# Kernel tuning notes

Measured on AMD Instinct MI355X. Metric: run time of the kernel, lower is better.

## Reference

```python
import jax, jax.numpy as jnp
import numpy as np

NEG = -1e9  # mask value for non-edges (matches masked_fill(-inf) numerically-safely)
SLOPE = 0.2  # LeakyReLU negative slope in GraphAttentionLayer


def gat_layer(x, W, a_l, a_r, adj, n_heads):
    """One GraphAttentionLayer (eval mode, is_concat=True).
    e[i,j,h] = leakyrelu(a_l . g[i,h] + a_r . g[j,h])  (attn Linear split into halves)
    softmax over j masked by adj, then aggregate neighbors.
    """
    n = x.shape[0]
    g = (x @ W).reshape(n, n_heads, -1)          # [n, h, f]
    el = jnp.einsum('ihf,f->ih', g, a_l)          # score contribution of node i
    er = jnp.einsum('jhf,f->jh', g, a_r)          # score contribution of node j
    e = jax.nn.leaky_relu(el[:, None, :] + er[None, :, :], SLOPE)  # [n, n, h]
    e = jnp.where(adj[:, :, None] != 0, e, NEG)
    a = jax.nn.softmax(e, axis=1)                 # softmax over neighbors j
    out = jnp.einsum('ijh,jhf->ihf', a, g)        # weighted aggregation
    return out.reshape(n, -1)                     # concat heads


def setup_inputs() -> dict:
    key = jax.random.key(0)
    ks = jax.random.split(key, 8)
    N, IN, HID, OUT, H = 2048, 512, 256, 128, 8
    x = jax.random.normal(ks[0], (N, IN), dtype=jnp.float32)
    adj = jax.random.randint(ks[1], (N, N), 0, 2, dtype=jnp.int32)
    adj = adj.at[jnp.arange(N), jnp.arange(N)].set(1)  # self loops: no empty softmax rows
    s = 0.05
    W1 = jax.random.normal(ks[2], (IN, HID), dtype=jnp.float32) * s
    a1_l = jax.random.normal(ks[3], (HID // H,), dtype=jnp.float32) * s
    a1_r = jax.random.normal(ks[4], (HID // H,), dtype=jnp.float32) * s
    W2 = jax.random.normal(ks[5], (HID, OUT), dtype=jnp.float32) * s
    a2_l = jax.random.normal(ks[6], (OUT,), dtype=jnp.float32) * s
    a2_r = jax.random.normal(ks[7], (OUT,), dtype=jnp.float32) * s
    return {"x": x, "W1": W1, "a1_l": a1_l, "a1_r": a1_r,
            "W2": W2, "a2_l": a2_l, "a2_r": a2_r, "adj_mat": adj}


def reference(x, W1, a1_l, a1_r, W2, a2_l, a2_r, adj_mat):
    # eval mode: nn.Dropout is identity
    h = gat_layer(x, W1, a1_l, a1_r, adj_mat, n_heads=8)
    h = jax.nn.elu(h)
    out = gat_layer(h, W2, a2_l, a2_r, adj_mat, n_heads=1)
    return out
```

## Files before the change

kernel.cpp:

```cpp
#include <hip/hip_runtime.h>
#include <hip/hip_bf16.h>

#define NN 2048
typedef unsigned short u16;
typedef unsigned long long u64;
typedef __attribute__((ext_vector_type(8))) short short8;
typedef __attribute__((ext_vector_type(4))) float f32x4;

__device__ __forceinline__ unsigned bfb(float x) {
    unsigned u = __float_as_uint(x);
    return (u + 0x7FFFu + ((u >> 16) & 1u)) >> 16;
}
__device__ __forceinline__ unsigned pk2(float a, float b) {
    unsigned r;
    asm("v_cvt_pk_bf16_f32 %0, %1, %2" : "=v"(r) : "v"(a), "v"(b));
    return r;
}

__global__ __launch_bounds__(256) void gemm1(const float* __restrict__ x,
                                             const float* __restrict__ W1,
                                             const int* __restrict__ adj,
                                             const float* __restrict__ al,
                                             const float* __restrict__ ar,
                                             u16* __restrict__ GT,
                                             float* __restrict__ el,
                                             float* __restrict__ ert,
                                             u64* __restrict__ ab) {
    const int rt = blockIdx.x, cs = blockIdx.y;
    const int i0 = rt * 16;
    const int t = threadIdx.x, lane = t & 63, w = t >> 6;
    const int q = lane >> 4, n = lane & 15;
    const int ct = w & 1, kh = w >> 1;
    __shared__ __align__(16) u16 As[16][520];
    __shared__ __align__(16) u16 Bs[32][520];
    __shared__ float osh[2][16][16];
    __shared__ float pel[2][16], per_[2][16];

    const int b = cs * 128 + rt;
    const int u0 = b * 64 + w * 16;
    int av[16];
#pragma unroll
    for (int it = 0; it < 16; ++it) {
        int u = u0 + it;
        av[it] = adj[(size_t)(u >> 5) * NN + (u & 31) * 64 + lane];
    }

    {
        const float4* xs = (const float4*)(x + (size_t)i0 * 512);
#pragma unroll
        for (int j = 0; j < 8; ++j) {
            float4 v = xs[j * 256 + t];
            int off = (j * 256 + t) * 4;
            int r = off >> 9, k = off & 511;
            uint2 o;
            o.x = pk2(v.x, v.y);
            o.y = pk2(v.z, v.w);
            *(uint2*)&As[r][k ^ ((r & 7) << 3)] = o;
        }
    }
    {
        const int c4 = (t & 7) * 4, kq = t >> 3;
#pragma unroll 8
        for (int pass = 0; pass < 16; ++pass) {
            int k = pass * 32 + kq;
            float4 v = *(const float4*)(W1 + (size_t)k * 256 + cs * 32 + c4);
            Bs[c4 + 0][k ^ (((c4 + 0) & 7) << 3)] = (u16)bfb(v.x);
            Bs[c4 + 1][k ^ (((c4 + 1) & 7) << 3)] = (u16)bfb(v.y);
            Bs[c4 + 2][k ^ (((c4 + 2) & 7) << 3)] = (u16)bfb(v.z);
            Bs[c4 + 3][k ^ (((c4 + 3) & 7) << 3)] = (u16)bfb(v.w);
        }
    }
#pragma unroll
    for (int it = 0; it < 16; ++it) {
        u64 mk = __ballot(av[it] != 0);
        int u = u0 + it;
        if (lane == 0) ab[(size_t)(u >> 5) * 32 + (u & 31)] = mk;
    }
    __syncthreads();

    const int an = n, bn = ct * 16 + n;
    const int k0 = kh * 256 + q * 8;
    f32x4 acc = {0.f, 0.f, 0.f, 0.f};
#pragma unroll
    for (int ks = 0; ks < 8; ++ks) {
        short8 a = *(const short8*)&As[an][(k0 + ks * 32) ^ ((an & 7) << 3)];
        short8 bb = *(const short8*)&Bs[bn][(k0 + ks * 32) ^ ((bn & 7) << 3)];
        acc = __builtin_amdgcn_mfma_f32_16x16x32_bf16(a, bb, acc, 0, 0, 0);
    }
    if (kh == 1) {
#pragma unroll
        for (int r = 0; r < 4; ++r) osh[ct][q * 4 + r][n] = acc[r];
    }
    __syncthreads();
    if (kh == 0) {
#pragma unroll
        for (int r = 0; r < 4; ++r) acc[r] += osh[ct][q * 4 + r][n];
        uint2 g0;
        g0.x = pk2(acc[0], acc[1]);
        g0.y = pk2(acc[2], acc[3]);
        *(uint2*)&GT[(size_t)(cs * 32 + ct * 16 + n) * NN + i0 + q * 4] = g0;
        const float alv = al[ct * 16 + n], arv = ar[ct * 16 + n];
#pragma unroll
        for (int r = 0; r < 4; ++r) {
            float ve = acc[r] * alv, vr = acc[r] * arv;
#pragma unroll
            for (int off = 1; off <= 8; off <<= 1) {
                ve += __shfl_xor(ve, off);
                vr += __shfl_xor(vr, off);
            }
            if (n == 0) { pel[ct][q * 4 + r] = ve; per_[ct][q * 4 + r] = vr; }
        }
    }
    __syncthreads();
    if (t < 16) {
        el[(size_t)(i0 + t) * 8 + cs] = pel[0][t] + pel[1][t];
        ert[(size_t)cs * NN + i0 + t] = per_[0][t] + per_[1][t];
    }
}

__global__ __launch_bounds__(256) void gemm2(const u16* __restrict__ A,
                                             const float* __restrict__ W2,
                                             const float* __restrict__ al,
                                             const float* __restrict__ ar,
                                             u16* __restrict__ GT,
                                             float* __restrict__ el2p,
                                             float* __restrict__ er2p) {
    const int i0 = blockIdx.x * 16, cs = blockIdx.y;
    const int t = threadIdx.x, lane = t & 63, w = t >> 6;
    const int q = lane >> 4, n = lane & 15;
    const int ct = w & 1, kh = w >> 1;
    __shared__ __align__(16) u16 As[16][264];
    __shared__ __align__(16) u16 Bs[32][264];
    __shared__ float osh[2][16][16];
    __shared__ float pel[2][16], per_[2][16];

    {
        const uint2* hs = (const uint2*)(A + (size_t)i0 * 256);
#pragma unroll
        for (int j = 0; j < 4; ++j) {
            uint2 v = hs[j * 256 + t];
            int off = (j * 256 + t) * 4;
            int r = off >> 8, k = off & 255;
            *(uint2*)&As[r][k ^ ((r & 7) << 3)] = v;
        }
    }
    {
        const int c4 = (t & 7) * 4, kq = t >> 3;
#pragma unroll 8
        for (int pass = 0; pass < 8; ++pass) {
            int k = pass * 32 + kq;
            float4 v = *(const float4*)(W2 + (size_t)k * 128 + cs * 32 + c4);
            Bs[c4 + 0][k ^ (((c4 + 0) & 7) << 3)] = (u16)bfb(v.x);
            Bs[c4 + 1][k ^ (((c4 + 1) & 7) << 3)] = (u16)bfb(v.y);
            Bs[c4 + 2][k ^ (((c4 + 2) & 7) << 3)] = (u16)bfb(v.z);
            Bs[c4 + 3][k ^ (((c4 + 3) & 7) << 3)] = (u16)bfb(v.w);
        }
    }
    __syncthreads();

    const int an = n, bn = ct * 16 + n;
    const int k0 = kh * 128 + q * 8;
    f32x4 acc = {0.f, 0.f, 0.f, 0.f};
#pragma unroll
    for (int ks = 0; ks < 4; ++ks) {
        short8 a = *(const short8*)&As[an][(k0 + ks * 32) ^ ((an & 7) << 3)];
        short8 bb = *(const short8*)&Bs[bn][(k0 + ks * 32) ^ ((bn & 7) << 3)];
        acc = __builtin_amdgcn_mfma_f32_16x16x32_bf16(a, bb, acc, 0, 0, 0);
    }
    if (kh == 1) {
#pragma unroll
        for (int r = 0; r < 4; ++r) osh[ct][q * 4 + r][n] = acc[r];
    }
    __syncthreads();
    if (kh == 0) {
#pragma unroll
        for (int r = 0; r < 4; ++r) acc[r] += osh[ct][q * 4 + r][n];
        uint2 g0;
        g0.x = pk2(acc[0], acc[1]);
        g0.y = pk2(acc[2], acc[3]);
        *(uint2*)&GT[(size_t)(cs * 32 + ct * 16 + n) * NN + i0 + q * 4] = g0;
        const float alv = al[cs * 32 + ct * 16 + n], arv = ar[cs * 32 + ct * 16 + n];
#pragma unroll
        for (int r = 0; r < 4; ++r) {
            float ve = acc[r] * alv, vr = acc[r] * arv;
#pragma unroll
            for (int off = 1; off <= 8; off <<= 1) {
                ve += __shfl_xor(ve, off);
                vr += __shfl_xor(vr, off);
            }
            if (n == 0) { pel[ct][q * 4 + r] = ve; per_[ct][q * 4 + r] = vr; }
        }
    }
    __syncthreads();
    if (t < 16) {
        el2p[(size_t)cs * NN + i0 + t] = pel[0][t] + pel[1][t];
        er2p[(size_t)cs * NN + i0 + t] = per_[0][t] + per_[1][t];
    }
}

__global__ __launch_bounds__(512, 4) void attn1(const float* __restrict__ el,
                                                const float* __restrict__ ert,
                                                const unsigned* __restrict__ ab32,
                                                const u16* __restrict__ gbt,
                                                u16* __restrict__ hbb) {
    const int rt = blockIdx.x, sec = blockIdx.y;
    const int i0 = rt * 16, h0 = sec * 2;
    const int t = threadIdx.x, lane = t & 63, w = t >> 6;
    const int q = lane >> 4, n = lane & 15;
    const int m = t >> 5, jq = t & 31;
    const int hl = w >> 2, ch = (w >> 1) & 1, kf2 = w & 1;

    __shared__ u16 ersb[2][2048];
    __shared__ __align__(16) u16 pl[2][2][16][264];
    __shared__ unsigned absh[16][64];
    __shared__ float psum_sh[16][2];
    __shared__ float osh[2][2][16][16];
    __shared__ float wmax[2][8];
    __shared__ float mxsh[2];

    float4 v0 = *(const float4*)(ert + (size_t)h0 * NN + t * 4);
    float4 v1 = *(const float4*)(ert + (size_t)(h0 + 1) * NN + t * 4);
    uint2 c0, c1;
    c0.x = pk2(v0.x, v0.y); c0.y = pk2(v0.z, v0.w);
    c1.x = pk2(v1.x, v1.y); c1.y = pk2(v1.z, v1.w);
    *(uint2*)&ersb[0][t * 4] = c0;
    *(uint2*)&ersb[1][t * 4] = c1;
    float m0 = fmaxf(fmaxf(v0.x, v0.y), fmaxf(v0.z, v0.w));
    float m1 = fmaxf(fmaxf(v1.x, v1.y), fmaxf(v1.z, v1.w));
#pragma unroll
    for (int off = 32; off; off >>= 1) {
        m0 = fmaxf(m0, __shfl_xor(m0, off));
        m1 = fmaxf(m1, __shfl_xor(m1, off));
    }
    if (lane == 0) { wmax[0][w] = m0; wmax[1][w] = m1; }
    for (int c = t; c < 1024; c += 512)
        absh[c >> 6][c & 63] = ab32[(size_t)(i0 + (c >> 6)) * 64 + (c & 63)];
    __syncthreads();
    if (t < 2) {
        float mm = wmax[t][0];
#pragma unroll
        for (int ww = 1; ww < 8; ++ww) mm = fmaxf(mm, wmax[t][ww]);
        mxsh[t] = mm;
    }
    __syncthreads();

    float elv[2], mxv[2], ps[2];
#pragma unroll
    for (int h = 0; h < 2; ++h) {
        float e = el[(size_t)(i0 + m) * 8 + h0 + h];
        elv[h] = e;
        float mm = e + mxsh[h];
        mxv[h] = fmaxf(mm, 0.2f * mm);
        ps[h] = 0.f;
    }

    auto stage = [&](int tl, int nb) {
#pragma unroll
        for (int sub = 0; sub < 2; ++sub) {
            unsigned word = absh[m][tl * 8 + sub * 4 + (jq >> 3)];
            unsigned bits = (word >> ((jq & 7) * 4)) & 0xFu;
            const int jo = tl * 256 + sub * 128 + jq * 4;
            uint2 raw0 = *(const uint2*)&ersb[0][jo];
            uint2 raw1 = *(const uint2*)&ersb[1][jo];
#pragma unroll
            for (int h = 0; h < 2; ++h) {
                uint2 raw = h ? raw1 : raw0;
                float e0 = __uint_as_float(raw.x << 16);
                float e1 = __uint_as_float(raw.x & 0xFFFF0000u);
                float e2 = __uint_as_float(raw.y << 16);
                float e3 = __uint_as_float(raw.y & 0xFFFF0000u);
                float s0 = elv[h] + e0, s1 = elv[h] + e1, s2 = elv[h] + e2, s3 = elv[h] + e3;
                s0 = fmaxf(s0, 0.2f * s0) - mxv[h];
                s1 = fmaxf(s1, 0.2f * s1) - mxv[h];
                s2 = fmaxf(s2, 0.2f * s2) - mxv[h];
                s3 = fmaxf(s3, 0.2f * s3) - mxv[h];
                float p0 = (bits & 1u) ? __expf(s0) : 0.f;
                float p1 = (bits & 2u) ? __expf(s1) : 0.f;
                float p2 = (bits & 4u) ? __expf(s2) : 0.f;
                float p3 = (bits & 8u) ? __expf(s3) : 0.f;
                ps[h] += (p0 + p1) + (p2 + p3);
                uint2 pkv;
                pkv.x = pk2(p0, p1);
                pkv.y = pk2(p2, p3);
                *(uint2*)&pl[nb][h][m][sub * 128 + jq * 4] = pkv;
            }
        }
    };

    const int col = sec * 64 + hl * 32 + ch * 16 + n;
    const u16* gb = gbt + (size_t)col * NN + kf2 * 128 + q * 8;
    short8 bc0 = *(const short8*)gb;
    short8 bc1 = *(const short8*)(gb + 32);
    short8 bc2 = *(const short8*)(gb + 64);
    short8 bc3 = *(const short8*)(gb + 96);
    f32x4 acc = {0.f, 0.f, 0.f, 0.f};

    stage(0, 0);
    __syncthreads();

    for (int tile = 0; tile < 8; ++tile) {
        short8 bn0 = bc0, bn1 = bc1, bn2 = bc2, bn3 = bc3;
        if (tile < 7) {
            const u16* gq = gb + (tile + 1) * 256;
            bn0 = *(const short8*)gq;
            bn1 = *(const short8*)(gq + 32);
            bn2 = *(const short8*)(gq + 64);
            bn3 = *(const short8*)(gq + 96);
        }
        const u16* ap = &pl[tile & 1][hl][n][kf2 * 128 + q * 8];
        short8 a0 = *(const short8*)ap;
        short8 a1 = *(const short8*)(ap + 32);
        short8 a2 = *(const short8*)(ap + 64);
        short8 a3 = *(const short8*)(ap + 96);
        acc = __builtin_amdgcn_mfma_f32_16x16x32_bf16(a0, bc0, acc, 0, 0, 0);
        acc = __builtin_amdgcn_mfma_f32_16x16x32_bf16(a1, bc1, acc, 0, 0, 0);
        acc = __builtin_amdgcn_mfma_f32_16x16x32_bf16(a2, bc2, acc, 0, 0, 0);
        acc = __builtin_amdgcn_mfma_f32_16x16x32_bf16(a3, bc3, acc, 0, 0, 0);
        if (tile < 7) stage(tile + 1, (tile + 1) & 1);
        bc0 = bn0; bc1 = bn1; bc2 = bn2; bc3 = bn3;
        __syncthreads();
    }

#pragma unroll
    for (int h = 0; h < 2; ++h) {
        float v = ps[h];
#pragma unroll
        for (int off = 16; off; off >>= 1) v += __shfl_down(v, off, 32);
        if (jq == 0) psum_sh[m][h] = v;
    }
    if (kf2 == 1) {
#pragma unroll
        for (int r = 0; r < 4; ++r) osh[hl][ch][q * 4 + r][n] = acc[r];
    }
    __syncthreads();
    if (kf2 == 0) {
#pragma unroll
        for (int r = 0; r < 4; ++r) {
            int mr = q * 4 + r;
            float o = (acc[r] + osh[hl][ch][mr][n]) / psum_sh[mr][hl];
            o = o > 0.f ? o : (__expf(o) - 1.f);
            hbb[(size_t)(i0 + mr) * 256 + col] = (u16)bfb(o);
        }
    }
}

__global__ __launch_bounds__(512) void attn2(const float* __restrict__ el2p,
                                             const float* __restrict__ er2p,
                                             const unsigned* __restrict__ ab32,
                                             const u16* __restrict__ gbt,
                                             float* __restrict__ out) {
    const int rt = blockIdx.x, sec = blockIdx.y;
    const int i0 = rt * 16;
    const int t = threadIdx.x, lane = t & 63, w = t >> 6;
    const int q = lane >> 4, n = lane & 15;
    const int m = t >> 5, jq = t & 31;
    const int ct = w >> 1, kf2 = w & 1;

    __shared__ u16 ersb[2048];
    __shared__ __align__(16) u16 pl[2][16][264];
    __shared__ unsigned absh[16][64];
    __shared__ float psum_sh[16];
    __shared__ float osh[4][16][16];
    __shared__ float wmax[8];
    __shared__ float mxsh;

    float4 a0 = *(const float4*)(er2p + t * 4);
    float4 a1 = *(const float4*)(er2p + NN + t * 4);
    float4 a2 = *(const float4*)(er2p + 2 * NN + t * 4);
    float4 a3 = *(const float4*)(er2p + 3 * NN + t * 4);
    float4 v0;
    v0.x = ((a0.x + a1.x) + (a2.x + a3.x));
    v0.y = ((a0.y + a1.y) + (a2.y + a3.y));
    v0.z = ((a0.z + a1.z) + (a2.z + a3.z));
    v0.w = ((a0.w + a1.w) + (a2.w + a3.w));
    uint2 c0;
    c0.x = pk2(v0.x, v0.y); c0.y = pk2(v0.z, v0.w);
    *(uint2*)&ersb[t * 4] = c0;
    float m0 = fmaxf(fmaxf(v0.x, v0.y), fmaxf(v0.z, v0.w));
#pragma unroll
    for (int off = 32; off; off >>= 1) m0 = fmaxf(m0, __shfl_xor(m0, off));
    if (lane == 0) wmax[w] = m0;
    for (int c = t; c < 1024; c += 512)
        absh[c >> 6][c & 63] = ab32[(size_t)(i0 + (c >> 6)) * 64 + (c & 63)];
    __syncthreads();
    if (t == 0) {
        float mm = wmax[0];
#pragma unroll
        for (int ww = 1; ww < 8; ++ww) mm = fmaxf(mm, wmax[ww]);
        mxsh = mm;
    }
    __syncthreads();

    const float elv = el2p[i0 + m] + el2p[NN + i0 + m] + el2p[2 * NN + i0 + m] + el2p[3 * NN + i0 + m];
    float mm2 = elv + mxsh;
    const float mxv = fmaxf(mm2, 0.2f * mm2);
    float ps = 0.f;

    auto stage = [&](int tl, int nb) {
#pragma unroll
        for (int sub = 0; sub < 2; ++sub) {
            unsigned word = absh[m][tl * 8 + sub * 4 + (jq >> 3)];
            unsigned bits = (word >> ((jq & 7) * 4)) & 0xFu;
            const int jo = tl * 256 + sub * 128 + jq * 4;
            uint2 raw = *(const uint2*)&ersb[jo];
            float e0 = __uint_as_float(raw.x << 16);
            float e1 = __uint_as_float(raw.x & 0xFFFF0000u);
            float e2 = __uint_as_float(raw.y << 16);
            float e3 = __uint_as_float(raw.y & 0xFFFF0000u);
            float s0 = elv + e0, s1 = elv + e1, s2 = elv + e2, s3 = elv + e3;
            s0 = fmaxf(s0, 0.2f * s0) - mxv;
            s1 = fmaxf(s1, 0.2f * s1) - mxv;
            s2 = fmaxf(s2, 0.2f * s2) - mxv;
            s3 = fmaxf(s3, 0.2f * s3) - mxv;
            float p0 = (bits & 1u) ? __expf(s0) : 0.f;
            float p1 = (bits & 2u) ? __expf(s1) : 0.f;
            float p2 = (bits & 4u) ? __expf(s2) : 0.f;
            float p3 = (bits & 8u) ? __expf(s3) : 0.f;
            ps += (p0 + p1) + (p2 + p3);
            uint2 pkv;
            pkv.x = pk2(p0, p1);
            pkv.y = pk2(p2, p3);
            *(uint2*)&pl[nb][m][sub * 128 + jq * 4] = pkv;
        }
    };

    const int col = sec * 64 + ct * 16 + n;
    const u16* gb = gbt + (size_t)col * NN + kf2 * 128 + q * 8;
    short8 bc0 = *(const short8*)gb;
    short8 bc1 = *(const short8*)(gb + 32);
    short8 bc2 = *(const short8*)(gb + 64);
    short8 bc3 = *(const short8*)(gb + 96);
    f32x4 acc = {0.f, 0.f, 0.f, 0.f};

    stage(0, 0);
    __syncthreads();

    for (int tile = 0; tile < 8; ++tile) {
        short8 bn0 = bc0, bn1 = bc1, bn2 = bc2, bn3 = bc3;
        if (tile < 7) {
            const u16* gq = gb + (tile + 1) * 256;
            bn0 = *(const short8*)gq;
            bn1 = *(const short8*)(gq + 32);
            bn2 = *(const short8*)(gq + 64);
            bn3 = *(const short8*)(gq + 96);
        }
        const u16* ap = &pl[tile & 1][n][kf2 * 128 + q * 8];
        short8 a0v = *(const short8*)ap;
        short8 a1v = *(const short8*)(ap + 32);
        short8 a2v = *(const short8*)(ap + 64);
        short8 a3v = *(const short8*)(ap + 96);
        acc = __builtin_amdgcn_mfma_f32_16x16x32_bf16(a0v, bc0, acc, 0, 0, 0);
        acc = __builtin_amdgcn_mfma_f32_16x16x32_bf16(a1v, bc1, acc, 0, 0, 0);
        acc = __builtin_amdgcn_mfma_f32_16x16x32_bf16(a2v, bc2, acc, 0, 0, 0);
        acc = __builtin_amdgcn_mfma_f32_16x16x32_bf16(a3v, bc3, acc, 0, 0, 0);
        if (tile < 7) stage(tile + 1, (tile + 1) & 1);
        bc0 = bn0; bc1 = bn1; bc2 = bn2; bc3 = bn3;
        __syncthreads();
    }

#pragma unroll
    for (int off = 16; off; off >>= 1) ps += __shfl_down(ps, off, 32);
    if (jq == 0) psum_sh[m] = ps;
    if (kf2 == 1) {
#pragma unroll
        for (int r = 0; r < 4; ++r) osh[ct][q * 4 + r][n] = acc[r];
    }
    __syncthreads();
    if (kf2 == 0) {
#pragma unroll
        for (int r = 0; r < 4; ++r) {
            int mr = q * 4 + r;
            out[(size_t)(i0 + mr) * 128 + col] = (acc[r] + osh[ct][mr][n]) / psum_sh[mr];
        }
    }
}

extern "C" void kernel_launch(void* const* d_in, const int* in_sizes, int n_in,
                              void* d_out, int out_size, void* d_ws, size_t ws_size,
                              hipStream_t stream) {
    const float* x   = (const float*)d_in[0];
    const float* W1  = (const float*)d_in[1];
    const float* a1l = (const float*)d_in[2];
    const float* a1r = (const float*)d_in[3];
    const float* W2  = (const float*)d_in[4];
    const float* a2l = (const float*)d_in[5];
    const float* a2r = (const float*)d_in[6];
    const int* adj = (const int*)d_in[7];

    char* p = (char*)d_ws;
    unsigned* abits = (unsigned*)p;  p += (size_t)NN * 64 * 4;
    u16* gbt1  = (u16*)p;            p += (size_t)256 * NN * 2;
    u16* hbb   = (u16*)p;            p += (size_t)NN * 256 * 2;
    u16* gbt2  = (u16*)p;            p += (size_t)128 * NN * 2;
    float* el1 = (float*)p;          p += (size_t)NN * 8 * 4;
    float* ert1 = (float*)p;         p += (size_t)8 * NN * 4;
    float* el2p = (float*)p;         p += (size_t)4 * NN * 4;
    float* er2p = (float*)p;         p += (size_t)4 * NN * 4;

    gemm1<<<dim3(128, 8), 256, 0, stream>>>(x, W1, adj, a1l, a1r, gbt1, el1, ert1, (u64*)abits);
    attn1<<<dim3(128, 4), 512, 0, stream>>>(el1, ert1, abits, gbt1, hbb);

    gemm2<<<dim3(128, 4), 256, 0, stream>>>(hbb, W2, a2l, a2r, gbt2, el2p, er2p);
    attn2<<<dim3(128, 2), 512, 0, stream>>>(el2p, er2p, abits, gbt2, (float*)d_out);
}
```

Baseline: 123.8 us.

## Drop adjacency bitmask precompute, read int adj directly in attention; XCD-aware block mapping

Removes the ballot-based bitmask packing of the adjacency matrix in gemm1, so each attention kernel reads the raw int32 adjacency rows directly and builds the 4-bit masks in registers. Adds an XCD-aware remapping of block indices so that blocks sharing rows or sections land on the same chiplet's L2. It also folds log2(e) into the attention vectors so the softmax can use the raw v_exp_f32 instead of __expf. The trade is reading 16 MB of int adjacency in each of the two attention kernels, instead of a 0.5 MB bitmask, in exchange for removing the mask-building pass from gemm1.

```diff
diff --git a/kernel.cpp b/kernel.cpp
--- a/kernel.cpp
+++ b/kernel.cpp
@@ -16,17 +16,24 @@
     asm("v_cvt_pk_bf16_f32 %0, %1, %2" : "=v"(r) : "v"(a), "v"(b));
     return r;
 }
+__device__ __forceinline__ float ex2(float x) {
+    float r;
+    asm("v_exp_f32 %0, %1" : "=v"(r) : "v"(x));
+    return r;
+}
+
+#define LOG2E 1.4426950408889634f
 
 __global__ __launch_bounds__(256) void gemm1(const float* __restrict__ x,
                                              const float* __restrict__ W1,
-                                             const int* __restrict__ adj,
                                              const float* __restrict__ al,
                                              const float* __restrict__ ar,
                                              u16* __restrict__ GT,
                                              float* __restrict__ el,
-                                             float* __restrict__ ert,
-                                             u64* __restrict__ ab) {
-    const int rt = blockIdx.x, cs = blockIdx.y;
+                                             float* __restrict__ ert) {
+    const int bid = blockIdx.x;
+    const int xcd = bid & 7, idx = bid >> 3;
+    const int rt = xcd * 16 + (idx & 15), cs = idx >> 4;
     const int i0 = rt * 16;
     const int t = threadIdx.x, lane = t & 63, w = t >> 6;
     const int q = lane >> 4, n = lane & 15;
@@ -36,22 +43,13 @@
     __shared__ float osh[2][16][16];
     __shared__ float pel[2][16], per_[2][16];
 
-    const int b = cs * 128 + rt;
-    const int u0 = b * 64 + w * 16;
-    int av[16];
-#pragma unroll
-    for (int it = 0; it < 16; ++it) {
-        int u = u0 + it;
-        av[it] = adj[(size_t)(u >> 5) * NN + (u & 31) * 64 + lane];
-    }
-
     {
         const float4* xs = (const float4*)(x + (size_t)i0 * 512);
 #pragma unroll
         for (int j = 0; j < 8; ++j) {
             float4 v = xs[j * 256 + t];
-            int off = (j * 256 + t) * 4;
-            int r = off >> 9, k = off & 511;
+            int e = (j * 256 + t) * 4;
+            int r = e >> 9, k = e & 511;
             uint2 o;
             o.x = pk2(v.x, v.y);
             o.y = pk2(v.z, v.w);
@@ -70,12 +68,6 @@
             Bs[c4 + 3][k ^ (((c4 + 3) & 7) << 3)] = (u16)bfb(v.w);
         }
     }
-#pragma unroll
-    for (int it = 0; it < 16; ++it) {
-        u64 mk = __ballot(av[it] != 0);
-        int u = u0 + it;
-        if (lane == 0) ab[(size_t)(u >> 5) * 32 + (u & 31)] = mk;
-    }
     __syncthreads();
 
     const int an = n, bn = ct * 16 + n;
@@ -99,7 +91,7 @@
         g0.x = pk2(acc[0], acc[1]);
         g0.y = pk2(acc[2], acc[3]);
         *(uint2*)&GT[(size_t)(cs * 32 + ct * 16 + n) * NN + i0 + q * 4] = g0;
-        const float alv = al[ct * 16 + n], arv = ar[ct * 16 + n];
+        const float alv = al[ct * 16 + n] * LOG2E, arv = ar[ct * 16 + n] * LOG2E;
 #pragma unroll
         for (int r = 0; r < 4; ++r) {
             float ve = acc[r] * alv, vr = acc[r] * arv;
@@ -139,8 +131,8 @@
 #pragma unroll
         for (int j = 0; j < 4; ++j) {
             uint2 v = hs[j * 256 + t];
-            int off = (j * 256 + t) * 4;
-            int r = off >> 8, k = off & 255;
+            int e = (j * 256 + t) * 4;
+            int r = e >> 8, k = e & 255;
             *(uint2*)&As[r][k ^ ((r & 7) << 3)] = v;
         }
     }
@@ -179,7 +171,7 @@
         g0.x = pk2(acc[0], acc[1]);
         g0.y = pk2(acc[2], acc[3]);
         *(uint2*)&GT[(size_t)(cs * 32 + ct * 16 + n) * NN + i0 + q * 4] = g0;
-        const float alv = al[cs * 32 + ct * 16 + n], arv = ar[cs * 32 + ct * 16 + n];
+        const float alv = al[cs * 32 + ct * 16 + n] * LOG2E, arv = ar[cs * 32 + ct * 16 + n] * LOG2E;
 #pragma unroll
         for (int r = 0; r < 4; ++r) {
             float ve = acc[r] * alv, vr = acc[r] * arv;
@@ -200,10 +192,13 @@
 
 __global__ __launch_bounds__(512, 4) void attn1(const float* __restrict__ el,
                                                 const float* __restrict__ ert,
-                                                const unsigned* __restrict__ ab32,
+                                                const int* __restrict__ adj,
                                                 const u16* __restrict__ gbt,
                                                 u16* __restrict__ hbb) {
-    const int rt = blockIdx.x, sec = blockIdx.y;
+    const int bid = blockIdx.x;
+    const int xcd = bid & 7, idx = bid >> 3;
+    const int sec = xcd >> 1;
+    const int rt = (xcd & 1) * 64 + idx;
     const int i0 = rt * 16, h0 = sec * 2;
     const int t = threadIdx.x, lane = t & 63, w = t >> 6;
     const int q = lane >> 4, n = lane & 15;
@@ -212,7 +207,6 @@
 
     __shared__ u16 ersb[2][2048];
     __shared__ __align__(16) u16 pl[2][2][16][264];
-    __shared__ unsigned absh[16][64];
     __shared__ float psum_sh[16][2];
     __shared__ float osh[2][2][16][16];
     __shared__ float wmax[2][8];
@@ -233,8 +227,6 @@
         m1 = fmaxf(m1, __shfl_xor(m1, off));
     }
     if (lane == 0) { wmax[0][w] = m0; wmax[1][w] = m1; }
-    for (int c = t; c < 1024; c += 512)
-        absh[c >> 6][c & 63] = ab32[(size_t)(i0 + (c >> 6)) * 64 + (c & 63)];
     __syncthreads();
     if (t < 2) {
         float mm = wmax[t][0];
@@ -253,12 +245,16 @@
         mxv[h] = fmaxf(mm, 0.2f * mm);
         ps[h] = 0.f;
     }
+    const int* adjrow = adj + (size_t)(i0 + m) * NN;
 
     auto stage = [&](int tl, int nb) {
+        int4 av0 = *(const int4*)(adjrow + tl * 256 + jq * 4);
+        int4 av1 = *(const int4*)(adjrow + tl * 256 + 128 + jq * 4);
 #pragma unroll
         for (int sub = 0; sub < 2; ++sub) {
-            unsigned word = absh[m][tl * 8 + sub * 4 + (jq >> 3)];
-            unsigned bits = (word >> ((jq & 7) * 4)) & 0xFu;
+            int4 av = sub ? av1 : av0;
+            unsigned bits = (unsigned)(av.x != 0) | ((unsigned)(av.y != 0) << 1) |
+                            ((unsigned)(av.z != 0) << 2) | ((unsigned)(av.w != 0) << 3);
             const int jo = tl * 256 + sub * 128 + jq * 4;
             uint2 raw0 = *(const uint2*)&ersb[0][jo];
             uint2 raw1 = *(const uint2*)&ersb[1][jo];
@@ -274,10 +270,10 @@
                 s1 = fmaxf(s1, 0.2f * s1) - mxv[h];
                 s2 = fmaxf(s2, 0.2f * s2) - mxv[h];
                 s3 = fmaxf(s3, 0.2f * s3) - mxv[h];
-                float p0 = (bits & 1u) ? __expf(s0) : 0.f;
-                float p1 = (bits & 2u) ? __expf(s1) : 0.f;
-                float p2 = (bits & 4u) ? __expf(s2) : 0.f;
-                float p3 = (bits & 8u) ? __expf(s3) : 0.f;
+                float p0 = (bits & 1u) ? ex2(s0) : 0.f;
+                float p1 = (bits & 2u) ? ex2(s1) : 0.f;
+                float p2 = (bits & 4u) ? ex2(s2) : 0.f;
+                float p3 = (bits & 8u) ? ex2(s3) : 0.f;
                 ps[h] += (p0 + p1) + (p2 + p3);
                 uint2 pkv;
                 pkv.x = pk2(p0, p1);
@@ -346,10 +342,13 @@
 
 __global__ __launch_bounds__(512) void attn2(const float* __restrict__ el2p,
                                              const float* __restrict__ er2p,
-                                             const unsigned* __restrict__ ab32,
+                                             const int* __restrict__ adj,
                                              const u16* __restrict__ gbt,
                                              float* __restrict__ out) {
-    const int rt = blockIdx.x, sec = blockIdx.y;
+    const int bid = blockIdx.x;
+    const int xcd = bid & 7, idx = bid >> 3;
+    const int sec = xcd >> 2;
+    const int rt = (xcd & 3) * 32 + idx;
     const int i0 = rt * 16;
     const int t = threadIdx.x, lane = t & 63, w = t >> 6;
     const int q = lane >> 4, n = lane & 15;
@@ -358,7 +357,6 @@
 
     __shared__ u16 ersb[2048];
     __shared__ __align__(16) u16 pl[2][16][264];
-    __shared__ unsigned absh[16][64];
     __shared__ float psum_sh[16];
     __shared__ float osh[4][16][16];
     __shared__ float wmax[8];
@@ -380,8 +378,6 @@
 #pragma unroll
     for (int off = 32; off; off >>= 1) m0 = fmaxf(m0, __shfl_xor(m0, off));
     if (lane == 0) wmax[w] = m0;
-    for (int c = t; c < 1024; c += 512)
-        absh[c >> 6][c & 63] = ab32[(size_t)(i0 + (c >> 6)) * 64 + (c & 63)];
     __syncthreads();
     if (t == 0) {
         float mm = wmax[0];
@@ -395,12 +391,16 @@
     float mm2 = elv + mxsh;
     const float mxv = fmaxf(mm2, 0.2f * mm2);
     float ps = 0.f;
+    const int* adjrow = adj + (size_t)(i0 + m) * NN;
 
     auto stage = [&](int tl, int nb) {
+        int4 av0 = *(const int4*)(adjrow + tl * 256 + jq * 4);
+        int4 av1 = *(const int4*)(adjrow + tl * 256 + 128 + jq * 4);
 #pragma unroll
         for (int sub = 0; sub < 2; ++sub) {
-            unsigned word = absh[m][tl * 8 + sub * 4 + (jq >> 3)];
-            unsigned bits = (word >> ((jq & 7) * 4)) & 0xFu;
+            int4 av = sub ? av1 : av0;
+            unsigned bits = (unsigned)(av.x != 0) | ((unsigned)(av.y != 0) << 1) |
+                            ((unsigned)(av.z != 0) << 2) | ((unsigned)(av.w != 0) << 3);
             const int jo = tl * 256 + sub * 128 + jq * 4;
             uint2 raw = *(const uint2*)&ersb[jo];
             float e0 = __uint_as_float(raw.x << 16);
@@ -412,10 +412,10 @@
             s1 = fmaxf(s1, 0.2f * s1) - mxv;
             s2 = fmaxf(s2, 0.2f * s2) - mxv;
             s3 = fmaxf(s3, 0.2f * s3) - mxv;
-            float p0 = (bits & 1u) ? __expf(s0) : 0.f;
-            float p1 = (bits & 2u) ? __expf(s1) : 0.f;
-            float p2 = (bits & 4u) ? __expf(s2) : 0.f;
-            float p3 = (bits & 8u) ? __expf(s3) : 0.f;
+            float p0 = (bits & 1u) ? ex2(s0) : 0.f;
+            float p1 = (bits & 2u) ? ex2(s1) : 0.f;
+            float p2 = (bits & 4u) ? ex2(s2) : 0.f;
+            float p3 = (bits & 8u) ? ex2(s3) : 0.f;
             ps += (p0 + p1) + (p2 + p3);
             uint2 pkv;
             pkv.x = pk2(p0, p1);
@@ -488,7 +488,6 @@
     const int* adj = (const int*)d_in[7];
 
     char* p = (char*)d_ws;
-    unsigned* abits = (unsigned*)p;  p += (size_t)NN * 64 * 4;
     u16* gbt1  = (u16*)p;            p += (size_t)256 * NN * 2;
     u16* hbb   = (u16*)p;            p += (size_t)NN * 256 * 2;
     u16* gbt2  = (u16*)p;            p += (size_t)128 * NN * 2;
@@ -497,9 +496,9 @@
     float* el2p = (float*)p;         p += (size_t)4 * NN * 4;
     float* er2p = (float*)p;         p += (size_t)4 * NN * 4;
 
-    gemm1<<<dim3(128, 8), 256, 0, stream>>>(x, W1, adj, a1l, a1r, gbt1, el1, ert1, (u64*)abits);
-    attn1<<<dim3(128, 4), 512, 0, stream>>>(el1, ert1, abits, gbt1, hbb);
+    gemm1<<<1024, 256, 0, stream>>>(x, W1, a1l, a1r, gbt1, el1, ert1);
+    attn1<<<512, 512, 0, stream>>>(el1, ert1, adj, gbt1, hbb);
 
     gemm2<<<dim3(128, 4), 256, 0, stream>>>(hbb, W2, a2l, a2r, gbt2, el2p, er2p);
-    attn2<<<dim3(128, 2), 512, 0, stream>>>(el2p, er2p, abits, gbt2, (float*)d_out);
-}
+    attn2<<<256, 512, 0, stream>>>(el2p, er2p, adj, gbt2, (float*)d_out);
+}
```

Measured after the change: 158.4 us. 27.9% more time.
